# Kernel tuning notes

Measured on AMD Instinct MI355X. Metric: run time of the kernel, lower is better.

Reference implementation:

```python
import jax, jax.numpy as jnp
import numpy as np

K = 8
DIM = 64
NUM_BLOCKS = 12
BN_EPS = 1e-5
LRELU_SLOPE = 0.01  # torch nn.LeakyReLU default negative_slope


def knn_indices(xyz, k):
    # xyz: [b, 3, n] -> idx [b, n, k] of k nearest neighbors (self included)
    x = jnp.transpose(xyz, (0, 2, 1))  # [b, n, 3]
    sq = jnp.sum(x * x, axis=-1)  # [b, n]
    d2 = sq[:, :, None] - 2.0 * jnp.einsum('bnd,bmd->bnm', x, x) + sq[:, None, :]
    _, idx = jax.lax.top_k(-d2, k)  # k smallest distances
    return idx


def group_point(points, idx):
    # points [b, d, n], idx [b, n, k] -> grouped [b, d, k, n]
    g = jax.vmap(lambda p, i: p[:, i])(points, idx)  # [b, d, n, k]
    return jnp.transpose(g, (0, 1, 3, 2))


def setup_inputs() -> dict:
    key = jax.random.key(0)
    ks = jax.random.split(key, 6)
    b, n = 8, 4096
    xyz = jax.random.normal(ks[0], (b, 3, n), dtype=jnp.float32)
    points = jax.random.normal(ks[1], (b, DIM, n), dtype=jnp.float32)
    # per-block params (note: the module's second Conv2d per block is never used
    # in forward — layers[4*idx+2] is applied to both center and grouped points)
    conv_w = jax.random.normal(ks[2], (NUM_BLOCKS, DIM, DIM), dtype=jnp.float32) * (1.0 / np.sqrt(DIM))
    conv_b = jax.random.normal(ks[3], (NUM_BLOCKS, DIM), dtype=jnp.float32) * 0.01
    bn_gamma = 1.0 + 0.1 * jax.random.normal(ks[4], (NUM_BLOCKS, DIM), dtype=jnp.float32)
    bn_beta = 0.1 * jax.random.normal(ks[5], (NUM_BLOCKS, DIM), dtype=jnp.float32)
    return {"xyz": xyz, "points": points, "conv_w": conv_w, "conv_b": conv_b,
            "bn_gamma": bn_gamma, "bn_beta": bn_beta}


def reference(xyz, points, conv_w, conv_b, bn_gamma, bn_beta):
    idx = knn_indices(xyz, K)  # fixed graph, computed once in block 0

    def block(p, params):
        w, b, g, be = params  # [DIM,DIM], [DIM], [DIM], [DIM]
        shortcut = p
        # BatchNorm1d (training-mode batch stats over batch & point dims)
        mean = jnp.mean(p, axis=(0, 2), keepdims=True)
        var = jnp.var(p, axis=(0, 2), keepdims=True)
        h = (p - mean) * jax.lax.rsqrt(var + BN_EPS) * g[None, :, None] + be[None, :, None]
        # LeakyReLU
        h = jnp.where(h >= 0, h, LRELU_SLOPE * h)
        # gather neighbor features: [b, d, k, n]
        grouped = group_point(h, idx)
        # shared 1x1 conv on center and grouped points
        center = jnp.einsum('od,bdn->bon', w, h) + b[None, :, None]            # [b,d,n]
        gconv = jnp.einsum('od,bdkn->bokn', w, grouped) + b[None, :, None, None]  # [b,d,k,n]
        # mean over concat([center[:, :, None], gconv], axis=2) == (center + sum_k gconv) / (k+1)
        new_p = (center + jnp.sum(gconv, axis=2)) / (K + 1) + shortcut
        return new_p, None

    out, _ = jax.lax.scan(block, points, (conv_w, conv_b, bn_gamma, bn_beta))
    return out
```

## Files before the change

### kernel.cpp

```cpp
#include <hip/hip_runtime.h>
#include <hip/hip_bf16.h>

#define NB     8
#define NPTS   4096
#define DIMC   64
#define KNN_K  8
#define NBLK   12
#define NREP   8

__global__ void zero_stats_kernel(float* __restrict__ stats) {
    int i = threadIdx.x + blockIdx.x * 256;
    if (i < 13 * NREP * 128) stats[i] = 0.0f;
}

__global__ __launch_bounds__(256) void prep_kernel(
        const float* __restrict__ xyz, float4* __restrict__ pts4g) {
#pragma clang fp contract(off)
    int g = blockIdx.x * 256 + threadIdx.x;
    int b = g >> 12, j = g & 4095;
    const float* xb = xyz + (size_t)b * 3 * NPTS;
    float x = xb[j];
    float y = xb[NPTS + j];
    float z = xb[2 * NPTS + j];
    float sq = (x * x + y * y) + z * z;
    pts4g[g] = make_float4(x, y, z, sq);
}

__global__ __launch_bounds__(256) void cast_kernel(
        const float* __restrict__ pts,
        float* __restrict__ P0, float* __restrict__ stats0) {
    __shared__ __align__(16) float tr[64 * 65];
    __shared__ float slotA[4 * 64], slotB[4 * 64];
    int wg = blockIdx.x;
    int b = wg & 7;
    int n0 = (wg >> 3) << 6;
    int rep = (wg >> 3) & (NREP - 1);
    int tid = threadIdx.x;
    int lane6 = tid & 63;
    int grp = tid >> 6;

    #pragma unroll
    for (int k = 0; k < 16; ++k) {
        int d = grp + (k << 2);
        float v = pts[(((size_t)((b << 6) + d)) << 12) + n0 + lane6];
        tr[d * 65 + lane6] = v;
    }
    __syncthreads();
    int c = lane6;
    float s = 0.0f, s2 = 0.0f;
    #pragma unroll
    for (int k = 0; k < 16; ++k) {
        int p = grp + (k << 2);
        float v = tr[c * 65 + p];
        P0[((size_t)((b << 12) + n0 + p)) * 64 + c] = v;
        s += v; s2 += v * v;
    }
    slotA[grp * 64 + c] = s;
    slotB[grp * 64 + c] = s2;
    __syncthreads();
    if (tid < 64) {
        float t = slotA[tid] + slotA[64 + tid] + slotA[128 + tid] + slotA[192 + tid];
        atomicAdd(&stats0[rep * 128 + tid], t);
    } else if (tid < 128) {
        int cc = tid - 64;
        float t = slotB[cc] + slotB[64 + cc] + slotB[128 + cc] + slotB[192 + cc];
        atomicAdd(&stats0[rep * 128 + 64 + cc], t);
    }
}

__global__ __launch_bounds__(512) void knn_kernel(
        const float4* __restrict__ pts4g, int* __restrict__ idx) {
#pragma clang fp contract(off)
    __shared__ __align__(16) float4 cand[2048];
    __shared__ double stash[4 * 9 * 128];
    int wg = blockIdx.x;
    int b = wg >> 5;
    int q0 = (wg & 31) << 7;
    int tid = threadIdx.x;

    int lane  = tid & 63;
    int wave  = tid >> 6;
    int chunk = wave & 3;
    int qgrp  = wave >> 2;
    int q_l   = (qgrp << 6) | lane;

    const float4* cb = pts4g + ((size_t)b << 12);
    float4 qp = cb[q0 + q_l];

    double k0, k1, k2, k3, k4, k5, k6, k7;
    k0 = k1 = k2 = k3 = k4 = k5 = k6 = k7 = __builtin_inf();
    float bd7f = 3.4e38f;

    for (int half = 0; half < 2; ++half) {
        if (half) __syncthreads();
        #pragma unroll
        for (int k = 0; k < 4; ++k)
            cand[tid + (k << 9)] = cb[(half << 11) + tid + (k << 9)];
        __syncthreads();

        int jl0 = chunk << 9;
        int jg0 = (half << 11) | (chunk << 9);
        int jstart = 0;

        if (half == 0) {
            for (int jo = 0; jo < 128; jo += 8) {
                float d2v[8];
                #pragma unroll
                for (int u = 0; u < 8; ++u) {
                    float4 p = cand[jl0 + jo + u];
                    float dot = (qp.x * p.x + qp.y * p.y) + qp.z * p.z;
                    d2v[u] = (qp.w - 2.0f * dot) + p.w;
                }
                #pragma unroll
                for (int u = 0; u < 8; ++u) {
                    unsigned long long kb =
                        __double_as_longlong((double)d2v[u]) |
                        (unsigned long long)(jg0 + jo + u);
                    double key = __longlong_as_double(kb);
                    double n0 = fmin(k0, key);
                    double n1 = fmin(k1, fmax(k0, key));
                    double n2 = fmin(k2, fmax(k1, key));
                    double n3 = fmin(k3, fmax(k2, key));
                    double n4 = fmin(k4, fmax(k3, key));
                    double n5 = fmin(k5, fmax(k4, key));
                    double n6 = fmin(k6, fmax(k5, key));
                    double n7 = fmin(k7, fmax(k6, key));
                    k0 = n0; k1 = n1; k2 = n2; k3 = n3;
                    k4 = n4; k5 = n5; k6 = n6; k7 = n7;
                }
            }
            bd7f = (float)k7;
            jstart = 128;
        }

        for (int jo = jstart; jo < 512; jo += 8) {
            float d2v[8];
            unsigned hm = 0u;
            #pragma unroll
            for (int u = 0; u < 8; ++u) {
                float4 p = cand[jl0 + jo + u];
                float dot = (qp.x * p.x + qp.y * p.y) + qp.z * p.z;
                float d2 = (qp.w - 2.0f * dot) + p.w;
                d2v[u] = d2;
                hm |= (d2 < bd7f) ? (1u << u) : 0u;
            }
            while (__any(hm != 0u)) {
                if (hm) {
                    int u = __builtin_ctz(hm);
                    hm &= hm - 1u;
                    float t0 = (u & 1) ? d2v[1] : d2v[0];
                    float t1 = (u & 1) ? d2v[3] : d2v[2];
                    float t2 = (u & 1) ? d2v[5] : d2v[4];
                    float t3 = (u & 1) ? d2v[7] : d2v[6];
                    float s0 = (u & 2) ? t1 : t0;
                    float s1 = (u & 2) ? t3 : t2;
                    float d2 = (u & 4) ? s1 : s0;
                    unsigned long long kb =
                        __double_as_longlong((double)d2) |
                        (unsigned long long)(jg0 + jo + u);
                    double key = __longlong_as_double(kb);
                    double n0 = fmin(k0, key);
                    double n1 = fmin(k1, fmax(k0, key));
                    double n2 = fmin(k2, fmax(k1, key));
                    double n3 = fmin(k3, fmax(k2, key));
                    double n4 = fmin(k4, fmax(k3, key));
                    double n5 = fmin(k5, fmax(k4, key));
                    double n6 = fmin(k6, fmax(k5, key));
                    double n7 = fmin(k7, fmax(k6, key));
                    k0 = n0; k1 = n1; k2 = n2; k3 = n3;
                    k4 = n4; k5 = n5; k6 = n6; k7 = n7;
                }
            }
            bd7f = (float)k7;
        }
    }

    {
        double* S = &stash[(chunk * 9) * 128 + q_l];
        S[0 * 128] = k0; S[1 * 128] = k1; S[2 * 128] = k2; S[3 * 128] = k3;
        S[4 * 128] = k4; S[5 * 128] = k5; S[6 * 128] = k6; S[7 * 128] = k7;
        S[8 * 128] = __builtin_inf();
    }
    __syncthreads();

    if (tid < 128) {
        int h0 = 0, h1 = 0, h2 = 0, h3 = 0;
        int* op = idx + ((size_t)(b * NPTS + q0 + tid)) * 8;
        #pragma unroll
        for (int t = 0; t < 8; ++t) {
            double b0 = stash[(0 * 9 + h0) * 128 + tid];
            double b1 = stash[(1 * 9 + h1) * 128 + tid];
            double b2 = stash[(2 * 9 + h2) * 128 + tid];
            double b3 = stash[(3 * 9 + h3) * 128 + tid];
            double best = b0; int bc = 0;
            if (b1 < best) { best = b1; bc = 1; }
            if (b2 < best) { best = b2; bc = 2; }
            if (b3 < best) { best = b3; bc = 3; }
            h0 += (bc == 0); h1 += (bc == 1);
            h2 += (bc == 2); h3 += (bc == 3);
            op[t] = (int)(__double_as_longlong(best) & 0xFFFULL);
        }
    }
}

__global__ __launch_bounds__(256) void block_kernel(
        const float* __restrict__ Pin, float* __restrict__ Pout,
        const float* __restrict__ statsIn, float* __restrict__ statsOut,
        const float* __restrict__ Wp, const float* __restrict__ Bp,
        const float* __restrict__ Gp, const float* __restrict__ Betap,
        const int* __restrict__ gidx, float* __restrict__ dout, int last) {
    __shared__ __align__(16) float Wt[64 * 68];
    __shared__ __align__(16) float mt[64 * 68];
    __shared__ __align__(16) float selft[64 * 64];
    __shared__ __align__(16) int   idxl[64 * 8];
    __shared__ __align__(16) float scale_l[64], shift_l[64], bias_l[64];
    __shared__ float slot[4 * 128];

    int wg = blockIdx.x;
    int b = wg & 7;
    int n0 = (wg >> 3) << 6;
    int rep = (wg >> 3) & (NREP - 1);
    int tid = threadIdx.x;

    const float* Pb = Pin + (((size_t)b) << 18);

    if (tid < 128) {
        ((int4*)idxl)[tid] = ((const int4*)(gidx + ((size_t)(b * NPTS + n0)) * 8))[tid];
    }
    #pragma unroll
    for (int k = 0; k < 4; ++k) {
        int lin = tid + (k << 8);
        ((float4*)selft)[lin] = ((const float4*)&Pb[(size_t)n0 << 6])[lin];
    }
    #pragma unroll
    for (int k = 0; k < 16; ++k) {
        int lin = tid + (k << 8);
        int o = lin >> 6, d = lin & 63;
        Wt[d * 68 + o] = Wp[lin];
    }
    if (tid < 64) {
        int c = tid;
        float sum = 0.0f, sumsq = 0.0f;
        #pragma unroll
        for (int r = 0; r < NREP; ++r) {
            sum   += statsIn[r * 128 + c];
            sumsq += statsIn[r * 128 + 64 + c];
        }
        float mean = sum * (1.0f / 32768.0f);
        float var  = sumsq * (1.0f / 32768.0f) - mean * mean;
        float rs   = 1.0f / sqrtf(var + 1e-5f);
        float sc   = Gp[c] * rs;
        scale_l[c] = sc;
        shift_l[c] = Betap[c] - mean * sc;
        bias_l[c]  = Bp[c];
    }
    __syncthreads();

    {
        int cq = tid & 15;
        int pg = tid >> 4;
        int c4 = cq << 2;
        float4 sc4 = *(const float4*)&scale_l[c4];
        float4 sh4 = *(const float4*)&shift_l[c4];
        #pragma unroll
        for (int i = 0; i < 4; ++i) {
            int pt = (pg << 2) + i;
            int4 ja = *(const int4*)&idxl[pt * 8];
            int4 jb = *(const int4*)&idxl[pt * 8 + 4];
            float4 v[9];
            v[0] = *(const float4*)&selft[(pt << 6) + c4];
            v[1] = *(const float4*)&Pb[(((size_t)ja.x) << 6) + c4];
            v[2] = *(const float4*)&Pb[(((size_t)ja.y) << 6) + c4];
            v[3] = *(const float4*)&Pb[(((size_t)ja.z) << 6) + c4];
            v[4] = *(const float4*)&Pb[(((size_t)ja.w) << 6) + c4];
            v[5] = *(const float4*)&Pb[(((size_t)jb.x) << 6) + c4];
            v[6] = *(const float4*)&Pb[(((size_t)jb.y) << 6) + c4];
            v[7] = *(const float4*)&Pb[(((size_t)jb.z) << 6) + c4];
            v[8] = *(const float4*)&Pb[(((size_t)jb.w) << 6) + c4];
            float4 a = make_float4(0.f, 0.f, 0.f, 0.f);
            #pragma unroll
            for (int k = 0; k < 9; ++k) {
                float hx = v[k].x * sc4.x + sh4.x;
                float hy = v[k].y * sc4.y + sh4.y;
                float hz = v[k].z * sc4.z + sh4.z;
                float hw = v[k].w * sc4.w + sh4.w;
                a.x += fmaxf(hx, 0.01f * hx);
                a.y += fmaxf(hy, 0.01f * hy);
                a.z += fmaxf(hz, 0.01f * hz);
                a.w += fmaxf(hw, 0.01f * hw);
            }
            mt[(c4 + 0) * 68 + pt] = a.x * (1.0f / 9.0f);
            mt[(c4 + 1) * 68 + pt] = a.y * (1.0f / 9.0f);
            mt[(c4 + 2) * 68 + pt] = a.z * (1.0f / 9.0f);
            mt[(c4 + 3) * 68 + pt] = a.w * (1.0f / 9.0f);
        }
    }
    __syncthreads();

    int o0 = (tid & 15) << 2;
    int p0 = (tid >> 4) << 2;
    float4 acc[4];
    {
        float4 bias4 = *(const float4*)&bias_l[o0];
        acc[0] = bias4; acc[1] = bias4; acc[2] = bias4; acc[3] = bias4;
    }
    #pragma unroll
    for (int d = 0; d < 64; ++d) {
        float4 wv = *(const float4*)&Wt[d * 68 + o0];
        float4 a  = *(const float4*)&mt[d * 68 + p0];
        acc[0].x += wv.x * a.x; acc[0].y += wv.y * a.x; acc[0].z += wv.z * a.x; acc[0].w += wv.w * a.x;
        acc[1].x += wv.x * a.y; acc[1].y += wv.y * a.y; acc[1].z += wv.z * a.y; acc[1].w += wv.w * a.y;
        acc[2].x += wv.x * a.z; acc[2].y += wv.y * a.z; acc[2].z += wv.z * a.z; acc[2].w += wv.w * a.z;
        acc[3].x += wv.x * a.w; acc[3].y += wv.y * a.w; acc[3].z += wv.z * a.w; acc[3].w += wv.w * a.w;
    }

    #pragma unroll
    for (int j = 0; j < 4; ++j) {
        float4 r = *(const float4*)&selft[((p0 + j) << 6) + o0];
        acc[j].x += r.x; acc[j].y += r.y; acc[j].z += r.z; acc[j].w += r.w;
    }

    if (!last) {
        float* PbOut = Pout + ((((size_t)b) << 12) + n0) * 64;
        #pragma unroll
        for (int j = 0; j < 4; ++j)
            *(float4*)&PbOut[((size_t)(p0 + j)) * 64 + o0] = acc[j];

        float4 s, s2;
        s.x = acc[0].x + acc[1].x + acc[2].x + acc[3].x;
        s.y = acc[0].y + acc[1].y + acc[2].y + acc[3].y;
        s.z = acc[0].z + acc[1].z + acc[2].z + acc[3].z;
        s.w = acc[0].w + acc[1].w + acc[2].w + acc[3].w;
        s2.x = acc[0].x*acc[0].x + acc[1].x*acc[1].x + acc[2].x*acc[2].x + acc[3].x*acc[3].x;
        s2.y = acc[0].y*acc[0].y + acc[1].y*acc[1].y + acc[2].y*acc[2].y + acc[3].y*acc[3].y;
        s2.z = acc[0].z*acc[0].z + acc[1].z*acc[1].z + acc[2].z*acc[2].z + acc[3].z*acc[3].z;
        s2.w = acc[0].w*acc[0].w + acc[1].w*acc[1].w + acc[2].w*acc[2].w + acc[3].w*acc[3].w;
        #pragma unroll
        for (int m = 16; m <= 32; m <<= 1) {
            s.x += __shfl_xor(s.x, m, 64);  s.y += __shfl_xor(s.y, m, 64);
            s.z += __shfl_xor(s.z, m, 64);  s.w += __shfl_xor(s.w, m, 64);
            s2.x += __shfl_xor(s2.x, m, 64); s2.y += __shfl_xor(s2.y, m, 64);
            s2.z += __shfl_xor(s2.z, m, 64); s2.w += __shfl_xor(s2.w, m, 64);
        }
        if ((tid & 63) < 16) {
            int w = tid >> 6;
            slot[w * 128 + o0 + 0] = s.x;  slot[w * 128 + o0 + 1] = s.y;
            slot[w * 128 + o0 + 2] = s.z;  slot[w * 128 + o0 + 3] = s.w;
            slot[w * 128 + 64 + o0 + 0] = s2.x; slot[w * 128 + 64 + o0 + 1] = s2.y;
            slot[w * 128 + 64 + o0 + 2] = s2.z; slot[w * 128 + 64 + o0 + 3] = s2.w;
        }
        __syncthreads();
        if (tid < 128) {
            float t = slot[tid] + slot[128 + tid] + slot[256 + tid] + slot[384 + tid];
            atomicAdd(&statsOut[rep * 128 + tid], t);
        }
    } else {
        __syncthreads();
        float* stage = mt;
        #pragma unroll
        for (int j = 0; j < 4; ++j) {
            stage[(o0 + 0) * 64 + p0 + j] = acc[j].x;
            stage[(o0 + 1) * 64 + p0 + j] = acc[j].y;
            stage[(o0 + 2) * 64 + p0 + j] = acc[j].z;
            stage[(o0 + 3) * 64 + p0 + j] = acc[j].w;
        }
        __syncthreads();
        #pragma unroll
        for (int k = 0; k < 16; ++k) {
            int lin = tid + (k << 8);
            int o = lin >> 6, pt = lin & 63;
            dout[(((size_t)((b << 6) + o)) << 12) + n0 + pt] = stage[lin];
        }
    }
}

extern "C" void kernel_launch(void* const* d_in, const int* in_sizes, int n_in,
                              void* d_out, int out_size, void* d_ws, size_t ws_size,
                              hipStream_t stream) {
    const float* xyz    = (const float*)d_in[0];
    const float* pts    = (const float*)d_in[1];
    const float* conv_w = (const float*)d_in[2];
    const float* conv_b = (const float*)d_in[3];
    const float* gamma  = (const float*)d_in[4];
    const float* beta   = (const float*)d_in[5];
    float* out = (float*)d_out;

    char* ws = (char*)d_ws;
    float*  P0    = (float*)(ws);
    float*  P1    = (float*)(ws + (size_t)8 * 1024 * 1024);
    int*    idx   = (int*)  (ws + (size_t)16 * 1024 * 1024);
    float*  stats = (float*)(ws + (size_t)17 * 1024 * 1024);
    float4* pts4g = (float4*)(ws + (size_t)18 * 1024 * 1024);

    zero_stats_kernel<<<52, 256, 0, stream>>>(stats);
    prep_kernel<<<128, 256, 0, stream>>>(xyz, pts4g);
    cast_kernel<<<512, 256, 0, stream>>>(pts, P0, stats);
    knn_kernel<<<256, 512, 0, stream>>>(pts4g, idx);

    float* Pbuf[2] = {P0, P1};
    for (int t = 0; t < NBLK; ++t) {
        block_kernel<<<512, 256, 0, stream>>>(
            Pbuf[t & 1], Pbuf[(t + 1) & 1],
            stats + (size_t)t * NREP * 128, stats + (size_t)(t + 1) * NREP * 128,
            conv_w + (size_t)t * 4096, conv_b + (size_t)t * 64,
            gamma + (size_t)t * 64, beta + (size_t)t * 64,
            idx, out, (t == NBLK - 1) ? 1 : 0);
    }
}
```

Measured before the change: 310.1 us.

## Fold stats zeroing into prep, stream KNN candidates from global, prefetch gathers

Stats zeroing moves into prep_kernel, which removes one kernel launch. The KNN kernel drops its shared-memory candidate staging and barriers, and each wave reads its 1024-candidate chunk directly from global memory through a wave-uniform pointer. This also changes the chunk layout from two halves of 512 to one contiguous chunk of 1024. In block_kernel the neighbor gathers are software-pipelined, so the next point's eight neighbor rows load while the current point accumulates. This adds register pressure and makes KNN rely on cache for candidate reuse.

```diff
diff --git a/kernel.cpp b/kernel.cpp
--- a/kernel.cpp
+++ b/kernel.cpp
@@ -8,15 +8,12 @@
 #define NBLK   12
 #define NREP   8
 
-__global__ void zero_stats_kernel(float* __restrict__ stats) {
-    int i = threadIdx.x + blockIdx.x * 256;
-    if (i < 13 * NREP * 128) stats[i] = 0.0f;
-}
-
 __global__ __launch_bounds__(256) void prep_kernel(
-        const float* __restrict__ xyz, float4* __restrict__ pts4g) {
+        const float* __restrict__ xyz, float4* __restrict__ pts4g,
+        float* __restrict__ stats) {
 #pragma clang fp contract(off)
     int g = blockIdx.x * 256 + threadIdx.x;
+    if (g < 13 * NREP * 128) stats[g] = 0.0f;
     int b = g >> 12, j = g & 4095;
     const float* xb = xyz + (size_t)b * 3 * NPTS;
     float x = xb[j];
@@ -68,10 +65,22 @@
     }
 }
 
+#define INS(KEY) do { \
+    double key = (KEY); \
+    double n0 = fmin(k0, key); \
+    double n1 = fmin(k1, fmax(k0, key)); \
+    double n2 = fmin(k2, fmax(k1, key)); \
+    double n3 = fmin(k3, fmax(k2, key)); \
+    double n4 = fmin(k4, fmax(k3, key)); \
+    double n5 = fmin(k5, fmax(k4, key)); \
+    double n6 = fmin(k6, fmax(k5, key)); \
+    double n7 = fmin(k7, fmax(k6, key)); \
+    k0 = n0; k1 = n1; k2 = n2; k3 = n3; \
+    k4 = n4; k5 = n5; k6 = n6; k7 = n7; } while (0)
+
 __global__ __launch_bounds__(512) void knn_kernel(
         const float4* __restrict__ pts4g, int* __restrict__ idx) {
 #pragma clang fp contract(off)
-    __shared__ __align__(16) float4 cand[2048];
     __shared__ double stash[4 * 9 * 128];
     int wg = blockIdx.x;
     int b = wg >> 5;
@@ -91,88 +100,57 @@
     k0 = k1 = k2 = k3 = k4 = k5 = k6 = k7 = __builtin_inf();
     float bd7f = 3.4e38f;
 
-    for (int half = 0; half < 2; ++half) {
-        if (half) __syncthreads();
-        #pragma unroll
-        for (int k = 0; k < 4; ++k)
-            cand[tid + (k << 9)] = cb[(half << 11) + tid + (k << 9)];
-        __syncthreads();
-
-        int jl0 = chunk << 9;
-        int jg0 = (half << 11) | (chunk << 9);
-        int jstart = 0;
-
-        if (half == 0) {
-            for (int jo = 0; jo < 128; jo += 8) {
-                float d2v[8];
-                #pragma unroll
-                for (int u = 0; u < 8; ++u) {
-                    float4 p = cand[jl0 + jo + u];
-                    float dot = (qp.x * p.x + qp.y * p.y) + qp.z * p.z;
-                    d2v[u] = (qp.w - 2.0f * dot) + p.w;
-                }
-                #pragma unroll
-                for (int u = 0; u < 8; ++u) {
-                    unsigned long long kb =
-                        __double_as_longlong((double)d2v[u]) |
-                        (unsigned long long)(jg0 + jo + u);
-                    double key = __longlong_as_double(kb);
-                    double n0 = fmin(k0, key);
-                    double n1 = fmin(k1, fmax(k0, key));
-                    double n2 = fmin(k2, fmax(k1, key));
-                    double n3 = fmin(k3, fmax(k2, key));
-                    double n4 = fmin(k4, fmax(k3, key));
-                    double n5 = fmin(k5, fmax(k4, key));
-                    double n6 = fmin(k6, fmax(k5, key));
-                    double n7 = fmin(k7, fmax(k6, key));
-                    k0 = n0; k1 = n1; k2 = n2; k3 = n3;
-                    k4 = n4; k5 = n5; k6 = n6; k7 = n7;
-                }
+    int chu = __builtin_amdgcn_readfirstlane(chunk);
+    const float4* cc = cb + ((size_t)chu << 10);
+    int jg0 = chu << 10;
+
+    for (int jo = 0; jo < 128; jo += 8) {
+        float d2v[8];
+        #pragma unroll
+        for (int u = 0; u < 8; ++u) {
+            float4 p = cc[jo + u];
+            float dot = (qp.x * p.x + qp.y * p.y) + qp.z * p.z;
+            d2v[u] = (qp.w - 2.0f * dot) + p.w;
+        }
+        #pragma unroll
+        for (int u = 0; u < 8; ++u) {
+            unsigned long long kb =
+                __double_as_longlong((double)d2v[u]) |
+                (unsigned long long)(jg0 + jo + u);
+            INS(__longlong_as_double(kb));
+        }
+    }
+    bd7f = (float)k7;
+
+    for (int jo = 128; jo < 1024; jo += 8) {
+        float d2v[8];
+        unsigned hm = 0u;
+        #pragma unroll
+        for (int u = 0; u < 8; ++u) {
+            float4 p = cc[jo + u];
+            float dot = (qp.x * p.x + qp.y * p.y) + qp.z * p.z;
+            float d2 = (qp.w - 2.0f * dot) + p.w;
+            d2v[u] = d2;
+            hm |= (d2 < bd7f) ? (1u << u) : 0u;
+        }
+        while (__any(hm != 0u)) {
+            if (hm) {
+                int u = __builtin_ctz(hm);
+                hm &= hm - 1u;
+                float t0 = (u & 1) ? d2v[1] : d2v[0];
+                float t1 = (u & 1) ? d2v[3] : d2v[2];
+                float t2 = (u & 1) ? d2v[5] : d2v[4];
+                float t3 = (u & 1) ? d2v[7] : d2v[6];
+                float s0 = (u & 2) ? t1 : t0;
+                float s1 = (u & 2) ? t3 : t2;
+                float d2 = (u & 4) ? s1 : s0;
+                unsigned long long kb =
+                    __double_as_longlong((double)d2) |
+                    (unsigned long long)(jg0 + jo + u);
+                INS(__longlong_as_double(kb));
             }
-            bd7f = (float)k7;
-            jstart = 128;
-        }
-
-        for (int jo = jstart; jo < 512; jo += 8) {
-            float d2v[8];
-            unsigned hm = 0u;
-            #pragma unroll
-            for (int u = 0; u < 8; ++u) {
-                float4 p = cand[jl0 + jo + u];
-                float dot = (qp.x * p.x + qp.y * p.y) + qp.z * p.z;
-                float d2 = (qp.w - 2.0f * dot) + p.w;
-                d2v[u] = d2;
-                hm |= (d2 < bd7f) ? (1u << u) : 0u;
-            }
-            while (__any(hm != 0u)) {
-                if (hm) {
-                    int u = __builtin_ctz(hm);
-                    hm &= hm - 1u;
-                    float t0 = (u & 1) ? d2v[1] : d2v[0];
-                    float t1 = (u & 1) ? d2v[3] : d2v[2];
-                    float t2 = (u & 1) ? d2v[5] : d2v[4];
-                    float t3 = (u & 1) ? d2v[7] : d2v[6];
-                    float s0 = (u & 2) ? t1 : t0;
-                    float s1 = (u & 2) ? t3 : t2;
-                    float d2 = (u & 4) ? s1 : s0;
-                    unsigned long long kb =
-                        __double_as_longlong((double)d2) |
-                        (unsigned long long)(jg0 + jo + u);
-                    double key = __longlong_as_double(kb);
-                    double n0 = fmin(k0, key);
-                    double n1 = fmin(k1, fmax(k0, key));
-                    double n2 = fmin(k2, fmax(k1, key));
-                    double n3 = fmin(k3, fmax(k2, key));
-                    double n4 = fmin(k4, fmax(k3, key));
-                    double n5 = fmin(k5, fmax(k4, key));
-                    double n6 = fmin(k6, fmax(k5, key));
-                    double n7 = fmin(k7, fmax(k6, key));
-                    k0 = n0; k1 = n1; k2 = n2; k3 = n3;
-                    k4 = n4; k5 = n5; k6 = n6; k7 = n7;
-                }
-            }
-            bd7f = (float)k7;
-        }
+        }
+        bd7f = (float)k7;
     }
 
     {
@@ -203,6 +181,16 @@
     }
 }
 
+#define ACC9(v) { \
+    float hx = (v).x * sc4.x + sh4.x; \
+    float hy = (v).y * sc4.y + sh4.y; \
+    float hz = (v).z * sc4.z + sh4.z; \
+    float hw = (v).w * sc4.w + sh4.w; \
+    a.x += fmaxf(hx, 0.01f * hx); \
+    a.y += fmaxf(hy, 0.01f * hy); \
+    a.z += fmaxf(hz, 0.01f * hz); \
+    a.w += fmaxf(hw, 0.01f * hw); }
+
 __global__ __launch_bounds__(256) void block_kernel(
         const float* __restrict__ Pin, float* __restrict__ Pout,
         const float* __restrict__ statsIn, float* __restrict__ statsOut,
@@ -262,37 +250,47 @@
         int c4 = cq << 2;
         float4 sc4 = *(const float4*)&scale_l[c4];
         float4 sh4 = *(const float4*)&shift_l[c4];
+        int ptb = pg << 2;
+
+        int4 ja = *(const int4*)&idxl[ptb * 8];
+        int4 jb = *(const int4*)&idxl[ptb * 8 + 4];
+        float4 n1 = *(const float4*)&Pb[(((size_t)ja.x) << 6) + c4];
+        float4 n2 = *(const float4*)&Pb[(((size_t)ja.y) << 6) + c4];
+        float4 n3 = *(const float4*)&Pb[(((size_t)ja.z) << 6) + c4];
+        float4 n4 = *(const float4*)&Pb[(((size_t)ja.w) << 6) + c4];
+        float4 n5 = *(const float4*)&Pb[(((size_t)jb.x) << 6) + c4];
+        float4 n6 = *(const float4*)&Pb[(((size_t)jb.y) << 6) + c4];
+        float4 n7 = *(const float4*)&Pb[(((size_t)jb.z) << 6) + c4];
+        float4 n8 = *(const float4*)&Pb[(((size_t)jb.w) << 6) + c4];
+
         #pragma unroll
         for (int i = 0; i < 4; ++i) {
-            int pt = (pg << 2) + i;
-            int4 ja = *(const int4*)&idxl[pt * 8];
-            int4 jb = *(const int4*)&idxl[pt * 8 + 4];
-            float4 v[9];
-            v[0] = *(const float4*)&selft[(pt << 6) + c4];
-            v[1] = *(const float4*)&Pb[(((size_t)ja.x) << 6) + c4];
-            v[2] = *(const float4*)&Pb[(((size_t)ja.y) << 6) + c4];
-            v[3] = *(const float4*)&Pb[(((size_t)ja.z) << 6) + c4];
-            v[4] = *(const float4*)&Pb[(((size_t)ja.w) << 6) + c4];
-            v[5] = *(const float4*)&Pb[(((size_t)jb.x) << 6) + c4];
-            v[6] = *(const float4*)&Pb[(((size_t)jb.y) << 6) + c4];
-            v[7] = *(const float4*)&Pb[(((size_t)jb.z) << 6) + c4];
-            v[8] = *(const float4*)&Pb[(((size_t)jb.w) << 6) + c4];
+            int pt = ptb + i;
+            float4 w1, w2, w3, w4, w5, w6, w7, w8;
+            if (i < 3) {
+                int4 ka = *(const int4*)&idxl[(pt + 1) * 8];
+                int4 kb = *(const int4*)&idxl[(pt + 1) * 8 + 4];
+                w1 = *(const float4*)&Pb[(((size_t)ka.x) << 6) + c4];
+                w2 = *(const float4*)&Pb[(((size_t)ka.y) << 6) + c4];
+                w3 = *(const float4*)&Pb[(((size_t)ka.z) << 6) + c4];
+                w4 = *(const float4*)&Pb[(((size_t)ka.w) << 6) + c4];
+                w5 = *(const float4*)&Pb[(((size_t)kb.x) << 6) + c4];
+                w6 = *(const float4*)&Pb[(((size_t)kb.y) << 6) + c4];
+                w7 = *(const float4*)&Pb[(((size_t)kb.z) << 6) + c4];
+                w8 = *(const float4*)&Pb[(((size_t)kb.w) << 6) + c4];
+            }
+            float4 v0 = *(const float4*)&selft[(pt << 6) + c4];
             float4 a = make_float4(0.f, 0.f, 0.f, 0.f);
-            #pragma unroll
-            for (int k = 0; k < 9; ++k) {
-                float hx = v[k].x * sc4.x + sh4.x;
-                float hy = v[k].y * sc4.y + sh4.y;
-                float hz = v[k].z * sc4.z + sh4.z;
-                float hw = v[k].w * sc4.w + sh4.w;
-                a.x += fmaxf(hx, 0.01f * hx);
-                a.y += fmaxf(hy, 0.01f * hy);
-                a.z += fmaxf(hz, 0.01f * hz);
-                a.w += fmaxf(hw, 0.01f * hw);
-            }
+            ACC9(v0); ACC9(n1); ACC9(n2); ACC9(n3); ACC9(n4);
+            ACC9(n5); ACC9(n6); ACC9(n7); ACC9(n8);
             mt[(c4 + 0) * 68 + pt] = a.x * (1.0f / 9.0f);
             mt[(c4 + 1) * 68 + pt] = a.y * (1.0f / 9.0f);
             mt[(c4 + 2) * 68 + pt] = a.z * (1.0f / 9.0f);
             mt[(c4 + 3) * 68 + pt] = a.w * (1.0f / 9.0f);
+            if (i < 3) {
+                n1 = w1; n2 = w2; n3 = w3; n4 = w4;
+                n5 = w5; n6 = w6; n7 = w7; n8 = w8;
+            }
         }
     }
     __syncthreads();
@@ -392,8 +390,7 @@
     float*  stats = (float*)(ws + (size_t)17 * 1024 * 1024);
     float4* pts4g = (float4*)(ws + (size_t)18 * 1024 * 1024);
 
-    zero_stats_kernel<<<52, 256, 0, stream>>>(stats);
-    prep_kernel<<<128, 256, 0, stream>>>(xyz, pts4g);
+    prep_kernel<<<128, 256, 0, stream>>>(xyz, pts4g, stats);
     cast_kernel<<<512, 256, 0, stream>>>(pts, P0, stats);
     knn_kernel<<<256, 512, 0, stream>>>(pts4g, idx);
 
```

New measurement: 313.1 us. No clear change (+1.0%).
